# Performance work log

Hardware: AMD Instinct MI355X
Metric: run time of the kernel (lower is better)

## Reference

```python
import jax, jax.numpy as jnp
import numpy as np

B, LP, NC, D, E = 8, 1000, 64, 128, 320  # batch, protein len, compound atoms, hid dim, esm dim


def _linear_params(key, din, dout):
    k1, k2 = jax.random.split(key)
    lim = 1.0 / np.sqrt(din)
    W = jax.random.uniform(k1, (din, dout), minval=-lim, maxval=lim, dtype=jnp.float32)
    b = jax.random.uniform(k2, (dout,), minval=-lim, maxval=lim, dtype=jnp.float32)
    return W, b


def setup_inputs() -> dict:
    key = jax.random.key(0)
    ks = jax.random.split(key, 14)
    inp = {
        "protein_embedding": jax.random.normal(ks[0], (B, LP, E), dtype=jnp.float32),
        "protein_feat_x": jax.random.normal(ks[1], (B, LP, D), dtype=jnp.float32),
        "compound_feats": jax.random.normal(ks[2], (B, NC, D), dtype=jnp.float32),
    }
    layers = [("emb", E, D), ("wq", D, D), ("wk", D, D), ("wv", D, D), ("wo", D, D),
              ("jp", D, D), ("jc", D, D),
              ("c1", D, 1024), ("c2", 1024, 1024), ("c3", 1024, 256), ("c4", 256, 1)]
    for i, (name, din, dout) in enumerate(layers):
        W, b = _linear_params(ks[3 + i], din, dout)
        inp[name + "_w"] = W
        inp[name + "_b"] = b
    return inp


def reference(protein_embedding, protein_feat_x, compound_feats,
              emb_w, emb_b, wq_w, wq_b, wk_w, wk_b, wv_w, wv_b, wo_w, wo_b,
              jp_w, jp_b, jc_w, jc_b,
              c1_w, c1_b, c2_w, c2_b, c3_w, c3_b, c4_w, c4_b):
    # protein sequence embedding -> hid dim
    pe = protein_embedding @ emb_w + emb_b                      # [B, LP, D]
    # single-head cross attention: query = seq embedding, key/value = graph feats
    Q = pe @ wq_w + wq_b
    K = protein_feat_x @ wk_w + wk_b
    V = protein_feat_x @ wv_w + wv_b
    scale = jnp.sqrt(jnp.asarray(D, pe.dtype))                  # n_heads=1 -> head_dim=D
    attn = jax.nn.softmax(jnp.einsum('bqd,bkd->bqk', Q, K) / scale, axis=-1)
    protein_feats = jnp.einsum('bqk,bkd->bqd', attn, V) @ wo_w + wo_b  # [B, LP, D]

    # sigmoid bilinear joint attention over (protein residue, compound atom) pairs
    P = jax.nn.relu(protein_feats) @ jp_w + jp_b                # [B, LP, D]
    C = jax.nn.relu(compound_feats) @ jc_w + jc_b               # [B, NC, D]
    A = jax.nn.sigmoid(jnp.einsum('bid,bkd->bik', P, C))        # [B, LP, NC]
    A = A / jnp.sum(A, axis=(1, 2), keepdims=True)

    # tanh outer product (the costly 4D bikj intermediate) then weighted reduction
    cp = jnp.tanh(protein_feats[:, :, None, :] * compound_feats[:, None, :, :])  # [B, LP, NC, D]
    cp_embedding = jnp.einsum('bikd,bik->bd', cp, A)            # [B, D]

    # classifier MLP (dropout is eval-mode identity)
    h = jax.nn.relu(cp_embedding @ c1_w + c1_b)
    h = jax.nn.relu(h @ c2_w + c2_b)
    h = jax.nn.relu(h @ c3_w + c3_b)
    return h @ c4_w + c4_b                                      # [B, 1]
```

## Files before the change

### kernel.cpp

```cpp
#include <hip/hip_runtime.h>
#include <hip/hip_bf16.h>
#include <math.h>

#define LP 1000
#define NCMP 64
#define NSPLIT 4

typedef _Float16 f16;
typedef f16   v8h __attribute__((ext_vector_type(8)));
typedef float v4f __attribute__((ext_vector_type(4)));

__device__ __forceinline__ float rcp_fast(float x) { return __builtin_amdgcn_rcpf(x); }
__device__ __forceinline__ void fsplit(float x, f16& h, f16& l) {
    h = (f16)x; l = (f16)(x - (float)h);
}
__device__ __forceinline__ void fs8(const float4& f0, const float4& f1, v8h& h, v8h& l) {
    const float x[8] = {f0.x, f0.y, f0.z, f0.w, f1.x, f1.y, f1.z, f1.w};
    #pragma unroll
    for (int i = 0; i < 8; ++i) {
        f16 hh = (f16)x[i];
        h[i] = hh;
        l[i] = (f16)(x[i] - (float)hh);
    }
}

struct H4 { f16 a, b, c, d; };

__device__ __forceinline__ void gemm_core(float (*Ws)[128], float (*Xt)[36],
                                          const float* X, const float* W, const float* bias,
                                          float* Y, int K, int rowbase, bool relu_in)
{
    const int t  = threadIdx.x;
    const int r0 = (t >> 5) * 4;
    const int c0 = (t & 31) * 4;
    const int xr = t >> 3, xk = (t & 7) << 2;
    const int xrow = rowbase + xr;
    float4 xv = *(const float4*)(X + (long)xrow * K + xk);
    float4 wv[4];
    #pragma unroll
    for (int u = 0; u < 4; ++u) {
        int s = t + u * 256, r = s >> 5, cb = (s & 31) << 2;
        wv[u] = *(const float4*)(W + (long)r * 128 + cb);
    }
    float acc[4][4] = {};
    for (int k0 = 0; k0 < K; k0 += 32) {
        float4 xs = xv;
        if (relu_in) { xs.x = fmaxf(xs.x,0.f); xs.y = fmaxf(xs.y,0.f);
                       xs.z = fmaxf(xs.z,0.f); xs.w = fmaxf(xs.w,0.f); }
        Xt[xk+0][xr] = xs.x; Xt[xk+1][xr] = xs.y; Xt[xk+2][xr] = xs.z; Xt[xk+3][xr] = xs.w;
        #pragma unroll
        for (int u = 0; u < 4; ++u) {
            int s = t + u * 256, r = s >> 5, cb = (s & 31) << 2;
            *(float4*)&Ws[r][cb] = wv[u];
        }
        __syncthreads();
        if (k0 + 32 < K) {
            xv = *(const float4*)(X + (long)xrow * K + k0 + 32 + xk);
            #pragma unroll
            for (int u = 0; u < 4; ++u) {
                int s = t + u * 256, r = s >> 5, cb = (s & 31) << 2;
                wv[u] = *(const float4*)(W + (long)(k0 + 32 + r) * 128 + cb);
            }
        }
        #pragma unroll
        for (int kk = 0; kk < 32; ++kk) {
            float4 w4 = *(const float4*)&Ws[kk][c0];
            float4 x4 = *(const float4*)&Xt[kk][r0];
            acc[0][0] = fmaf(x4.x, w4.x, acc[0][0]); acc[0][1] = fmaf(x4.x, w4.y, acc[0][1]);
            acc[0][2] = fmaf(x4.x, w4.z, acc[0][2]); acc[0][3] = fmaf(x4.x, w4.w, acc[0][3]);
            acc[1][0] = fmaf(x4.y, w4.x, acc[1][0]); acc[1][1] = fmaf(x4.y, w4.y, acc[1][1]);
            acc[1][2] = fmaf(x4.y, w4.z, acc[1][2]); acc[1][3] = fmaf(x4.y, w4.w, acc[1][3]);
            acc[2][0] = fmaf(x4.z, w4.x, acc[2][0]); acc[2][1] = fmaf(x4.z, w4.y, acc[2][1]);
            acc[2][2] = fmaf(x4.z, w4.z, acc[2][2]); acc[2][3] = fmaf(x4.z, w4.w, acc[2][3]);
            acc[3][0] = fmaf(x4.w, w4.x, acc[3][0]); acc[3][1] = fmaf(x4.w, w4.y, acc[3][1]);
            acc[3][2] = fmaf(x4.w, w4.z, acc[3][2]); acc[3][3] = fmaf(x4.w, w4.w, acc[3][3]);
        }
        __syncthreads();
    }
    float4 bv = bias ? *(const float4*)(bias + c0) : make_float4(0.f,0.f,0.f,0.f);
    #pragma unroll
    for (int i = 0; i < 4; ++i) {
        int row = rowbase + r0 + i;
        float4 o;
        o.x = acc[i][0] + bv.x; o.y = acc[i][1] + bv.y;
        o.z = acc[i][2] + bv.z; o.w = acc[i][3] + bv.w;
        *(float4*)(Y + (long)row * 128 + c0) = o;
    }
}

__device__ __forceinline__ void gemm_coreT(float (*Ws)[128], float (*Xt)[36],
                                           const float* X, const float* W,
                                           f16* ThT, f16* TlT, int KT, int rowbase)
{
    const int t  = threadIdx.x;
    const int r0 = (t >> 5) * 4;
    const int c0 = (t & 31) * 4;
    const int xr = t >> 3, xk = (t & 7) << 2;
    const int xrow = rowbase + xr;
    float4 xv = *(const float4*)(X + (long)xrow * 128 + xk);
    float4 wv[4];
    #pragma unroll
    for (int u = 0; u < 4; ++u) {
        int s = t + u * 256, r = s >> 5, cb = (s & 31) << 2;
        wv[u] = *(const float4*)(W + (long)r * 128 + cb);
    }
    float acc[4][4] = {};
    for (int k0 = 0; k0 < 128; k0 += 32) {
        Xt[xk+0][xr] = xv.x; Xt[xk+1][xr] = xv.y; Xt[xk+2][xr] = xv.z; Xt[xk+3][xr] = xv.w;
        #pragma unroll
        for (int u = 0; u < 4; ++u) {
            int s = t + u * 256, r = s >> 5, cb = (s & 31) << 2;
            *(float4*)&Ws[r][cb] = wv[u];
        }
        __syncthreads();
        if (k0 + 32 < 128) {
            xv = *(const float4*)(X + (long)xrow * 128 + k0 + 32 + xk);
            #pragma unroll
            for (int u = 0; u < 4; ++u) {
                int s = t + u * 256, r = s >> 5, cb = (s & 31) << 2;
                wv[u] = *(const float4*)(W + (long)(k0 + 32 + r) * 128 + cb);
            }
        }
        #pragma unroll
        for (int kk = 0; kk < 32; ++kk) {
            float4 w4 = *(const float4*)&Ws[kk][c0];
            float4 x4 = *(const float4*)&Xt[kk][r0];
            acc[0][0] = fmaf(x4.x, w4.x, acc[0][0]); acc[0][1] = fmaf(x4.x, w4.y, acc[0][1]);
            acc[0][2] = fmaf(x4.x, w4.z, acc[0][2]); acc[0][3] = fmaf(x4.x, w4.w, acc[0][3]);
            acc[1][0] = fmaf(x4.y, w4.x, acc[1][0]); acc[1][1] = fmaf(x4.y, w4.y, acc[1][1]);
            acc[1][2] = fmaf(x4.y, w4.z, acc[1][2]); acc[1][3] = fmaf(x4.y, w4.w, acc[1][3]);
            acc[2][0] = fmaf(x4.z, w4.x, acc[2][0]); acc[2][1] = fmaf(x4.z, w4.y, acc[2][1]);
            acc[2][2] = fmaf(x4.z, w4.z, acc[2][2]); acc[2][3] = fmaf(x4.z, w4.w, acc[2][3]);
            acc[3][0] = fmaf(x4.w, w4.x, acc[3][0]); acc[3][1] = fmaf(x4.w, w4.y, acc[3][1]);
            acc[3][2] = fmaf(x4.w, w4.z, acc[3][2]); acc[3][3] = fmaf(x4.w, w4.w, acc[3][3]);
        }
        __syncthreads();
    }
    #pragma unroll
    for (int i = 0; i < 4; ++i) {
        int row = rowbase + r0 + i;
        #pragma unroll
        for (int j = 0; j < 4; ++j) {
            f16 h, l; fsplit(acc[i][j], h, l);
            long o = (long)(c0 + j) * KT + row;
            ThT[o] = h; TlT[o] = l;
        }
    }
}

__global__ __launch_bounds__(256) void pre0_k(const float* __restrict__ emb_w, const float* __restrict__ emb_b,
                                              const float* __restrict__ wq_w, const float* __restrict__ wq_b,
                                              const float* __restrict__ wk_w,
                                              const float* __restrict__ wv_w, const float* __restrict__ wv_b,
                                              const float* __restrict__ wo_w, const float* __restrict__ wo_b,
                                              f16* __restrict__ WpThi, f16* __restrict__ WpTlo,
                                              f16* __restrict__ WkThi, f16* __restrict__ WkTlo,
                                              float* __restrict__ bp,
                                              float* __restrict__ Wvo, float* __restrict__ bvo,
                                              float* __restrict__ zbase)
{
    __shared__ __align__(16) float Ws[32][128];
    __shared__ __align__(16) float Xt[32][36];
    const int bid = blockIdx.x;
    const int t = threadIdx.x;
    if (bid < 10) { gemm_coreT(Ws, Xt, emb_w, wq_w, WpThi, WpTlo, 320, bid * 32); return; }
    if (bid >= 11 && bid < 15) { gemm_core(Ws, Xt, wv_w, wo_w, nullptr, Wvo, 128, (bid - 11) * 32, false); return; }
    if (bid >= 16) {
        #pragma unroll
        for (int u = 0; u < 8; ++u) {
            int idx = (bid - 16) * 2048 + u * 256 + t;
            int k = idx >> 7, n = idx & 127;
            f16 h, l; fsplit(wk_w[idx], h, l);
            WkThi[(long)n * 128 + k] = h; WkTlo[(long)n * 128 + k] = l;
        }
        return;
    }
    if (bid == 10 && t >= 128) {
        for (int i = t - 128; i < 1032; i += 128) zbase[i] = 0.f;
        return;
    }
    if (t < 128) {
        const float* vb = (bid == 10) ? emb_b : wv_b;
        const float* Wm = (bid == 10) ? wq_w  : wo_w;
        const float* ab = (bid == 10) ? wq_b  : wo_b;
        float a0 = 0.f, a1 = 0.f, a2 = 0.f, a3 = 0.f;
        for (int k = 0; k < 128; k += 4) {
            a0 = fmaf(vb[k+0], Wm[(k+0)*128 + t], a0);
            a1 = fmaf(vb[k+1], Wm[(k+1)*128 + t], a1);
            a2 = fmaf(vb[k+2], Wm[(k+2)*128 + t], a2);
            a3 = fmaf(vb[k+3], Wm[(k+3)*128 + t], a3);
        }
        float* dst = (bid == 10) ? bp : bvo;
        dst[t] = (a0 + a1) + (a2 + a3) + ab[t];
    }
}

__global__ __launch_bounds__(256) void qkv3_k(
    const float* __restrict__ PE, const float* __restrict__ PFX,
    const f16* __restrict__ WpThi, const f16* __restrict__ WpTlo,
    const f16* __restrict__ WkThi, const f16* __restrict__ WkTlo,
    const float* __restrict__ bp, const float* __restrict__ wk_b,
    const float* __restrict__ CF, const float* __restrict__ jc_w, const float* __restrict__ jc_b,
    f16* __restrict__ Qhi, f16* __restrict__ Qlo,
    f16* __restrict__ Khi, f16* __restrict__ Klo,
    f16* __restrict__ Vthi, f16* __restrict__ Vtlo,
    float* __restrict__ Cj)
{
    __shared__ __align__(16) float Ws[32][128];
    __shared__ __align__(16) float Xt[32][36];
    const int bid = blockIdx.x;
    const int t = threadIdx.x;
    if (bid >= 272) {
        const int rb = (bid - 272) * 32;
        const int d = t >> 1, half = t & 1;
        #pragma unroll 4
        for (int i = 0; i < 16; ++i) {
            int row = rb + half * 16 + i;
            int bb = row / 1000, rr = row - bb * 1000;
            float v = PFX[(long)row * 128 + d];
            f16 h, l; fsplit(v, h, l);
            long o = ((long)bb * 128 + d) * 1024 + rr;
            Vthi[o] = h; Vtlo[o] = l;
        }
        return;
    }
    if (bid >= 256) { gemm_core(Ws, Xt, CF, jc_w, jc_b, Cj, 128, (bid - 256) * 32, true); return; }
    const bool isQ = bid < 128;
    const int b = (bid & 127) >> 4, tile = bid & 15;
    const int KD  = isQ ? 320 : 128;
    const int NCH = isQ ? 10 : 4;
    const float* A = isQ ? PE : PFX;
    const f16* Bhi = isQ ? WpThi : WkThi;
    const f16* Blo = isQ ? WpTlo : WkTlo;
    const float* bias = isQ ? bp : wk_b;
    f16* Yhi = isQ ? Qhi : Khi;
    f16* Ylo = isQ ? Qlo : Klo;

    const int wv = t >> 6, lane = t & 63, quad = lane >> 4, l4 = lane & 15;
    int arow = tile * 64 + wv * 16 + l4; if (arow >= LP) arow = LP - 1;
    const float* a_p = A + ((long)b * LP + arow) * KD;

    v4f acc[8];
    #pragma unroll
    for (int dt = 0; dt < 8; ++dt) acc[dt] = (v4f){0.f, 0.f, 0.f, 0.f};

    for (int kt = 0; kt < NCH; ++kt) {
        const int ko = kt * 32 + quad * 8;
        float4 f0 = *(const float4*)(a_p + ko);
        float4 f1 = *(const float4*)(a_p + ko + 4);
        v8h ah, al;
        fs8(f0, f1, ah, al);
        #pragma unroll
        for (int dt = 0; dt < 8; ++dt) {
            const long bo = (long)(dt * 16 + l4) * KD + ko;
            v8h bh = *(const v8h*)(Bhi + bo);
            v8h bl = *(const v8h*)(Blo + bo);
            acc[dt] = __builtin_amdgcn_mfma_f32_16x16x32_f16(ah, bh, acc[dt], 0, 0, 0);
            acc[dt] = __builtin_amdgcn_mfma_f32_16x16x32_f16(ah, bl, acc[dt], 0, 0, 0);
            acc[dt] = __builtin_amdgcn_mfma_f32_16x16x32_f16(al, bh, acc[dt], 0, 0, 0);
        }
    }
    #pragma unroll
    for (int dt = 0; dt < 8; ++dt) {
        const int col = dt * 16 + l4;
        const float bv = bias[col];
        #pragma unroll
        for (int r = 0; r < 4; ++r) {
            int row = tile * 64 + wv * 16 + quad * 4 + r;
            long o = ((long)b * 1024 + row) * 128 + col;
            f16 h, l; fsplit(acc[dt][r] + bv, h, l);
            Yhi[o] = h; Ylo[o] = l;
        }
    }
}

__global__ __launch_bounds__(256) void flash7_k(const f16* __restrict__ Qhi, const f16* __restrict__ Qlo,
                                                const f16* __restrict__ Khi, const f16* __restrict__ Klo,
                                                const f16* __restrict__ Vthi, const f16* __restrict__ Vtlo,
                                                float* __restrict__ Opart,
                                                float* __restrict__ mpart, float* __restrict__ lpart)
{
    __shared__ __align__(16) f16 KVhi[9216];
    __shared__ __align__(16) f16 KVlo[9216];
    __shared__ __align__(16) f16 Pshi[4][16 * 72];
    __shared__ __align__(16) f16 Pslo[4][16 * 72];
    const int t    = threadIdx.x;
    const int wv   = t >> 6;
    const int lane = t & 63;
    const int quad = lane >> 4;
    const int l4   = lane & 15;
    const int qt = blockIdx.x, sp = blockIdx.y, b = blockIdx.z;
    const int q0 = qt * 64;
    const float SCALE = 0.08838834764831845f;
    const float L2E   = 1.4426950408889634f;

    int qrow = q0 + wv * 16 + l4; if (qrow >= LP) qrow = LP - 1;
    const long qbase = ((long)b * 1024 + qrow) * 128;
    v8h qh[4], ql[4];
    #pragma unroll
    for (int kt4 = 0; kt4 < 4; ++kt4) {
        qh[kt4] = *(const v8h*)(Qhi + qbase + kt4 * 32 + quad * 8);
        ql[kt4] = *(const v8h*)(Qlo + qbase + kt4 * 32 + quad * 8);
    }
    float m_i[4] = { -3.0e38f, -3.0e38f, -3.0e38f, -3.0e38f };
    float l_i[4] = { 0.f, 0.f, 0.f, 0.f };
    v4f  O[8];
    #pragma unroll
    for (int dt = 0; dt < 8; ++dt) O[dt] = (v4f){0.f, 0.f, 0.f, 0.f};

    for (int kt = sp * 4; kt < sp * 4 + 4; ++kt) {
        const int key0 = kt * 64;
        __syncthreads();
        #pragma unroll
        for (int u = 0; u < 4; ++u) {
            int ch = t + u * 256;
            int r = ch >> 4, co = (ch & 15) * 8;
            long ga = ((long)b * 1024 + key0 + r) * 128 + co;
            *(v8h*)(KVhi + r * 136 + co) = *(const v8h*)(Khi + ga);
            *(v8h*)(KVlo + r * 136 + co) = *(const v8h*)(Klo + ga);
        }
        __syncthreads();
        v8h vh[4], vl[4];
        #pragma unroll
        for (int u = 0; u < 4; ++u) {
            int ch = t + u * 256;
            int d = ch >> 3, co = (ch & 7) * 8;
            long ga = ((long)b * 128 + d) * 1024 + key0 + co;
            vh[u] = *(const v8h*)(Vthi + ga);
            vl[u] = *(const v8h*)(Vtlo + ga);
        }
        v4f S[4];
        #pragma unroll
        for (int nt = 0; nt < 4; ++nt) S[nt] = (v4f){0.f, 0.f, 0.f, 0.f};
        #pragma unroll
        for (int nt = 0; nt < 4; ++nt) {
            const int rb = (nt * 16 + l4) * 136;
            #pragma unroll
            for (int kt4 = 0; kt4 < 4; ++kt4) {
                v8h bh = *(const v8h*)(KVhi + rb + kt4 * 32 + quad * 8);
                v8h bl = *(const v8h*)(KVlo + rb + kt4 * 32 + quad * 8);
                S[nt] = __builtin_amdgcn_mfma_f32_16x16x32_f16(qh[kt4], bh, S[nt], 0, 0, 0);
                S[nt] = __builtin_amdgcn_mfma_f32_16x16x32_f16(qh[kt4], bl, S[nt], 0, 0, 0);
                S[nt] = __builtin_amdgcn_mfma_f32_16x16x32_f16(ql[kt4], bh, S[nt], 0, 0, 0);
            }
        }
        #pragma unroll
        for (int nt = 0; nt < 4; ++nt) {
            bool valid = (key0 + nt * 16 + l4) < LP;
            #pragma unroll
            for (int r = 0; r < 4; ++r)
                S[nt][r] = valid ? S[nt][r] * SCALE : -3.0e38f;
        }
        float alpha[4];
        #pragma unroll
        for (int r = 0; r < 4; ++r) {
            float tm = fmaxf(fmaxf(S[0][r], S[1][r]), fmaxf(S[2][r], S[3][r]));
            tm = fmaxf(tm, __shfl_xor(tm, 1));
            tm = fmaxf(tm, __shfl_xor(tm, 2));
            tm = fmaxf(tm, __shfl_xor(tm, 4));
            tm = fmaxf(tm, __shfl_xor(tm, 8));
            float mnew = fmaxf(m_i[r], tm);
            alpha[r] = exp2f((m_i[r] - mnew) * L2E);
            float ps = 0.f;
            #pragma unroll
            for (int nt = 0; nt < 4; ++nt) {
                float p = exp2f((S[nt][r] - mnew) * L2E);
                S[nt][r] = p;
                ps += p;
            }
            ps += __shfl_xor(ps, 1);
            ps += __shfl_xor(ps, 2);
            ps += __shfl_xor(ps, 4);
            ps += __shfl_xor(ps, 8);
            l_i[r] = l_i[r] * alpha[r] + ps;
            m_i[r] = mnew;
        }
        #pragma unroll
        for (int dt = 0; dt < 8; ++dt) {
            O[dt][0] *= alpha[0]; O[dt][1] *= alpha[1];
            O[dt][2] *= alpha[2]; O[dt][3] *= alpha[3];
        }
        __syncthreads();
        #pragma unroll
        for (int u = 0; u < 4; ++u) {
            int ch = t + u * 256;
            int d = ch >> 3, co = (ch & 7) * 8;
            *(v8h*)(KVhi + d * 72 + co) = vh[u];
            *(v8h*)(KVlo + d * 72 + co) = vl[u];
        }
        #pragma unroll
        for (int nt = 0; nt < 4; ++nt) {
            int col = nt * 16 + l4;
            #pragma unroll
            for (int r = 0; r < 4; ++r) {
                f16 ph, pl; fsplit(S[nt][r], ph, pl);
                Pshi[wv][(quad * 4 + r) * 72 + col] = ph;
                Pslo[wv][(quad * 4 + r) * 72 + col] = pl;
            }
        }
        __syncthreads();
        #pragma unroll
        for (int kc = 0; kc < 2; ++kc) {
            v8h pah = *(const v8h*)(Pshi[wv] + l4 * 72 + kc * 32 + quad * 8);
            v8h pal = *(const v8h*)(Pslo[wv] + l4 * 72 + kc * 32 + quad * 8);
            #pragma unroll
            for (int dt = 0; dt < 8; ++dt) {
                v8h vfh = *(const v8h*)(KVhi + (dt * 16 + l4) * 72 + kc * 32 + quad * 8);
                v8h vfl = *(const v8h*)(KVlo + (dt * 16 + l4) * 72 + kc * 32 + quad * 8);
                O[dt] = __builtin_amdgcn_mfma_f32_16x16x32_f16(pah, vfh, O[dt], 0, 0, 0);
                O[dt] = __builtin_amdgcn_mfma_f32_16x16x32_f16(pah, vfl, O[dt], 0, 0, 0);
                O[dt] = __builtin_amdgcn_mfma_f32_16x16x32_f16(pal, vfh, O[dt], 0, 0, 0);
            }
        }
    }
    #pragma unroll
    for (int r = 0; r < 4; ++r) {
        int row = q0 + wv * 16 + quad * 4 + r;
        if (row < LP) {
            long base = (long)sp * 1024000 + ((long)b * LP + row) * 128;
            #pragma unroll
            for (int dt = 0; dt < 8; ++dt)
                Opart[base + dt * 16 + l4] = O[dt][r];
            if (l4 == 0) {
                mpart[(long)sp * 8000 + b * LP + row] = m_i[r];
                lpart[(long)sp * 8000 + b * LP + row] = l_i[r];
            }
        }
    }
}

__global__ __launch_bounds__(256) void mt1ab_k(
    const float* __restrict__ Opart, const float* __restrict__ mp, const float* __restrict__ lp,
    const float* __restrict__ Wvo, const float* __restrict__ bvo,
    const float* __restrict__ jp_w, const float* __restrict__ jp_b,
    float* __restrict__ PF, float* __restrict__ PJ)
{
    __shared__ __align__(16) float Ws[128][128];
    __shared__ __align__(16) float Xs[16][132];
    const int t  = threadIdx.x;
    const int p0 = blockIdx.x * 16;
    const int b  = blockIdx.y;
    const float L2E = 1.4426950408889634f;
    const int r0 = (t >> 5) * 2;
    const int c0 = (t & 31) * 4;

    #pragma unroll
    for (int u = 0; u < 16; ++u) {
        int s = t + u * 256, r = s >> 5, cb = (s & 31) << 2;
        *(float4*)&Ws[r][cb] = *(const float4*)(Wvo + (long)r * 128 + cb);
    }
    {
        const int pr = t >> 4, pc = (t & 15) << 3;
        int grow = p0 + pr; if (grow > LP - 1) grow = LP - 1;
        const long g = (long)b * LP + grow;
        float mm = -3.0e38f;
        #pragma unroll
        for (int s = 0; s < NSPLIT; ++s) mm = fmaxf(mm, mp[g + (long)s * 8000]);
        float wgt[NSPLIT]; float ls = 0.f;
        #pragma unroll
        for (int s = 0; s < NSPLIT; ++s) {
            wgt[s] = exp2f((mp[g + (long)s * 8000] - mm) * L2E);
            ls += wgt[s] * lp[g + (long)s * 8000];
        }
        const float linv = 1.0f / ls;
        float4 a0 = make_float4(0.f,0.f,0.f,0.f), a1 = make_float4(0.f,0.f,0.f,0.f);
        #pragma unroll
        for (int s = 0; s < NSPLIT; ++s) {
            const float* src = Opart + (long)s * 1024000 + g * 128 + pc;
            float4 p = *(const float4*)src;
            float4 q = *(const float4*)(src + 4);
            a0.x = fmaf(wgt[s], p.x, a0.x); a0.y = fmaf(wgt[s], p.y, a0.y);
            a0.z = fmaf(wgt[s], p.z, a0.z); a0.w = fmaf(wgt[s], p.w, a0.w);
            a1.x = fmaf(wgt[s], q.x, a1.x); a1.y = fmaf(wgt[s], q.y, a1.y);
            a1.z = fmaf(wgt[s], q.z, a1.z); a1.w = fmaf(wgt[s], q.w, a1.w);
        }
        *(float4*)&Xs[pr][pc]     = make_float4(a0.x*linv, a0.y*linv, a0.z*linv, a0.w*linv);
        *(float4*)&Xs[pr][pc + 4] = make_float4(a1.x*linv, a1.y*linv, a1.z*linv, a1.w*linv);
    }
    __syncthreads();
    float acc[2][4] = {};
    #pragma unroll 8
    for (int kk4 = 0; kk4 < 128; kk4 += 4) {
        float4 xa = *(const float4*)&Xs[r0 + 0][kk4];
        float4 xb = *(const float4*)&Xs[r0 + 1][kk4];
        #pragma unroll
        for (int j = 0; j < 4; ++j) {
            float4 w4 = *(const float4*)&Ws[kk4 + j][c0];
            float x0 = (j==0)?xa.x:(j==1)?xa.y:(j==2)?xa.z:xa.w;
            float x1 = (j==0)?xb.x:(j==1)?xb.y:(j==2)?xb.z:xb.w;
            acc[0][0]=fmaf(x0,w4.x,acc[0][0]); acc[0][1]=fmaf(x0,w4.y,acc[0][1]);
            acc[0][2]=fmaf(x0,w4.z,acc[0][2]); acc[0][3]=fmaf(x0,w4.w,acc[0][3]);
            acc[1][0]=fmaf(x1,w4.x,acc[1][0]); acc[1][1]=fmaf(x1,w4.y,acc[1][1]);
            acc[1][2]=fmaf(x1,w4.z,acc[1][2]); acc[1][3]=fmaf(x1,w4.w,acc[1][3]);
        }
    }
    __syncthreads();
    #pragma unroll
    for (int u = 0; u < 16; ++u) {
        int s = t + u * 256, r = s >> 5, cb = (s & 31) << 2;
        *(float4*)&Ws[r][cb] = *(const float4*)(jp_w + (long)r * 128 + cb);
    }
    {
        float4 bv = *(const float4*)(bvo + c0);
        #pragma unroll
        for (int i = 0; i < 2; ++i) {
            float4 o = make_float4(acc[i][0]+bv.x, acc[i][1]+bv.y, acc[i][2]+bv.z, acc[i][3]+bv.w);
            int orow = p0 + r0 + i;
            if (orow < LP)
                *(float4*)(PF + ((long)b * LP + orow) * 128 + c0) = o;
            *(float4*)&Xs[r0 + i][c0] =
                make_float4(fmaxf(o.x,0.f), fmaxf(o.y,0.f), fmaxf(o.z,0.f), fmaxf(o.w,0.f));
        }
    }
    __syncthreads();
    float ac2[2][4] = {};
    #pragma unroll 8
    for (int kk4 = 0; kk4 < 128; kk4 += 4) {
        float4 xa = *(const float4*)&Xs[r0 + 0][kk4];
        float4 xb = *(const float4*)&Xs[r0 + 1][kk4];
        #pragma unroll
        for (int j = 0; j < 4; ++j) {
            float4 w4 = *(const float4*)&Ws[kk4 + j][c0];
            float x0 = (j==0)?xa.x:(j==1)?xa.y:(j==2)?xa.z:xa.w;
            float x1 = (j==0)?xb.x:(j==1)?xb.y:(j==2)?xb.z:xb.w;
            ac2[0][0]=fmaf(x0,w4.x,ac2[0][0]); ac2[0][1]=fmaf(x0,w4.y,ac2[0][1]);
            ac2[0][2]=fmaf(x0,w4.z,ac2[0][2]); ac2[0][3]=fmaf(x0,w4.w,ac2[0][3]);
            ac2[1][0]=fmaf(x1,w4.x,ac2[1][0]); ac2[1][1]=fmaf(x1,w4.y,ac2[1][1]);
            ac2[1][2]=fmaf(x1,w4.z,ac2[1][2]); ac2[1][3]=fmaf(x1,w4.w,ac2[1][3]);
        }
    }
    float4 b2 = *(const float4*)(jp_b + c0);
    #pragma unroll
    for (int i = 0; i < 2; ++i) {
        int orow = p0 + r0 + i;
        if (orow < LP)
            *(float4*)(PJ + ((long)b * LP + orow) * 128 + c0) =
                make_float4(ac2[i][0]+b2.x, ac2[i][1]+b2.y, ac2[i][2]+b2.z, ac2[i][3]+b2.w);
    }
}

template<int IIN>
__device__ __forceinline__ float tanh_chunk(const float (*Cs)[132], const float (*AshT)[20],
                                            const float* areg, int d, int kh)
{
    float accD = 0.f;
    for (int kk = 0; kk < 16; ++kk) {
        const int k = (kh << 4) + kk;
        const float cv = Cs[k][d];
        #pragma unroll
        for (int iq = 0; iq < IIN; iq += 4) {
            float4 a4 = *(const float4*)&AshT[k][iq];
            float e0 = exp2f(areg[iq+0] * cv);
            float e1 = exp2f(areg[iq+1] * cv);
            float e2 = exp2f(areg[iq+2] * cv);
            float e3 = exp2f(areg[iq+3] * cv);
            accD = fmaf(1.f - 2.f * rcp_fast(e0 + 1.f), a4.x, accD);
            accD = fmaf(1.f - 2.f * rcp_fast(e1 + 1.f), a4.y, accD);
            accD = fmaf(1.f - 2.f * rcp_fast(e2 + 1.f), a4.z, accD);
            accD = fmaf(1.f - 2.f * rcp_fast(e3 + 1.f), a4.w, accD);
        }
    }
    return accD;
}

__global__ __launch_bounds__(256) void mt2_k(
    const float* __restrict__ PF, const float* __restrict__ PJ,
    const float* __restrict__ Cj, const float* __restrict__ CF,
    float* __restrict__ Asum, float* __restrict__ cpe)
{
    __shared__ __align__(16) float Pjs[16][132];
    __shared__ __align__(16) float Pfs[16][132];
    __shared__ __align__(16) float Cs[32][132];
    __shared__ __align__(16) float AshT[32][20];
    __shared__ float red[256];
    const int t  = threadIdx.x;
    const int p0 = blockIdx.x * 16;
    const int kc = blockIdx.y;
    const int b  = blockIdx.z;
    const float L2E = 1.4426950408889634f;

    {
        int pr = t >> 4, pc = (t & 15) << 3;
        int gr = p0 + pr; if (gr > LP - 1) gr = LP - 1;
        long gb = ((long)b * LP + gr) * 128 + pc;
        *(float4*)&Pjs[pr][pc]     = *(const float4*)(PJ + gb);
        *(float4*)&Pjs[pr][pc + 4] = *(const float4*)(PJ + gb + 4);
        *(float4*)&Pfs[pr][pc]     = *(const float4*)(PF + gb);
        *(float4*)&Pfs[pr][pc + 4] = *(const float4*)(PF + gb + 4);
    }
    float4 cfv[4];
    #pragma unroll
    for (int u = 0; u < 4; ++u) {
        int s = t + u * 256, r = s >> 5, cb = (s & 31) << 2;
        *(float4*)&Cs[r][cb] = *(const float4*)(Cj + ((long)b * NCMP + kc * 32 + r) * 128 + cb);
        cfv[u] = *(const float4*)(CF + ((long)b * NCMP + kc * 32 + r) * 128 + cb);
    }
    __syncthreads();
    const int tr = t >> 4, tc = t & 15;
    float sacc[2] = {0.f, 0.f};
    #pragma unroll 4
    for (int d4 = 0; d4 < 32; ++d4) {
        float4 p4 = *(const float4*)&Pjs[tr][d4 << 2];
        #pragma unroll
        for (int j = 0; j < 2; ++j) {
            float4 cv = *(const float4*)&Cs[tc + (j << 4)][d4 << 2];
            sacc[j] += p4.x*cv.x + p4.y*cv.y + p4.z*cv.z + p4.w*cv.w;
        }
    }
    float lsum = 0.f;
    const int gi = p0 + tr;
    #pragma unroll
    for (int j = 0; j < 2; ++j) {
        float sg = rcp_fast(1.f + exp2f(-sacc[j] * L2E));
        if (gi < LP) { AshT[tc + (j << 4)][tr] = sg; lsum += sg; }
    }
    #pragma unroll
    for (int off = 1; off < 64; off <<= 1) lsum += __shfl_xor(lsum, off);
    if ((t & 63) == 0) red[t >> 6] = lsum;
    __syncthreads();
    if (t == 0) atomicAdd(Asum + b, (red[0] + red[1]) + (red[2] + red[3]));
    #pragma unroll
    for (int u = 0; u < 4; ++u) {
        int s = t + u * 256, r = s >> 5, cb = (s & 31) << 2;
        *(float4*)&Cs[r][cb] = cfv[u];
    }
    __syncthreads();
    const float TWO_L2E = 2.8853900817779268f;
    const int d = t & 127, kh = t >> 7;
    float areg[16];
    #pragma unroll
    for (int ii = 0; ii < 16; ++ii) areg[ii] = Pfs[ii][d] * TWO_L2E;
    float accD = (p0 + 16 <= LP) ? tanh_chunk<16>(Cs, AshT, areg, d, kh)
                                 : tanh_chunk<8>(Cs, AshT, areg, d, kh);
    red[t] = accD;
    __syncthreads();
    if (t < 128) atomicAdd(cpe + (long)b * 128 + t, red[t] + red[t + 128]);
}

__global__ __launch_bounds__(256) void c12_k(const float* __restrict__ cpe, const float* __restrict__ Asum,
                                             const float* __restrict__ c1_w, const float* __restrict__ c1_b,
                                             const float* __restrict__ c2_w, float* __restrict__ part)
{
    __shared__ float sc[8][128];
    __shared__ float ins[8][8];
    const int t = threadIdx.x, ks = blockIdx.x, k0 = ks * 8;
    #pragma unroll
    for (int u = 0; u < 4; ++u) {
        int idx = t + u * 256;
        sc[idx >> 7][idx & 127] = cpe[idx] * rcp_fast(Asum[idx >> 7]);
    }
    __syncthreads();
    if (t < 64) {
        int b = t >> 3, kk = t & 7;
        int n1 = k0 + kk;
        float a0 = 0.f, a1 = 0.f, a2 = 0.f, a3 = 0.f;
        #pragma unroll 8
        for (int j = 0; j < 128; j += 4) {
            a0 = fmaf(sc[b][j+0], c1_w[(long)(j+0)*1024 + n1], a0);
            a1 = fmaf(sc[b][j+1], c1_w[(long)(j+1)*1024 + n1], a1);
            a2 = fmaf(sc[b][j+2], c1_w[(long)(j+2)*1024 + n1], a2);
            a3 = fmaf(sc[b][j+3], c1_w[(long)(j+3)*1024 + n1], a3);
        }
        ins[b][kk] = fmaxf((a0 + a1) + (a2 + a3) + c1_b[n1], 0.f);
    }
    __syncthreads();
    const int n = (t & 63) * 4 + (t >> 6) * 256;
    float4 acc[8] = {};
    #pragma unroll
    for (int kk = 0; kk < 8; ++kk) {
        float4 w4 = *(const float4*)(c2_w + (long)(k0 + kk) * 1024 + n);
        #pragma unroll
        for (int b = 0; b < 8; ++b) {
            float s = ins[b][kk];
            acc[b].x = fmaf(s, w4.x, acc[b].x); acc[b].y = fmaf(s, w4.y, acc[b].y);
            acc[b].z = fmaf(s, w4.z, acc[b].z); acc[b].w = fmaf(s, w4.w, acc[b].w);
        }
    }
    #pragma unroll
    for (int b = 0; b < 8; ++b)
        *(float4*)(part + ((long)(ks * 8 + b)) * 1024 + n) = acc[b];
}

__global__ __launch_bounds__(256) void c3m_k(const float* __restrict__ part2, const float* __restrict__ c2_b,
                                             const float* __restrict__ c3_w, const float* __restrict__ c3_b,
                                             const float* __restrict__ c4_w, const float* __restrict__ c4_b,
                                             float* __restrict__ out)
{
    __shared__ float Hs[1024];
    __shared__ float red[256];
    const int t = threadIdx.x, b = blockIdx.x;
    float4 acc4 = make_float4(0.f,0.f,0.f,0.f);
    #pragma unroll 4
    for (int ks = 0; ks < 128; ++ks) {
        float4 p = *(const float4*)(part2 + ((long)(ks * 8 + b)) * 1024 + t * 4);
        acc4.x += p.x; acc4.y += p.y; acc4.z += p.z; acc4.w += p.w;
    }
    {
        float4 bb = *(const float4*)(c2_b + t * 4);
        Hs[t*4+0] = fmaxf(acc4.x + bb.x, 0.f);
        Hs[t*4+1] = fmaxf(acc4.y + bb.y, 0.f);
        Hs[t*4+2] = fmaxf(acc4.z + bb.z, 0.f);
        Hs[t*4+3] = fmaxf(acc4.w + bb.w, 0.f);
    }
    __syncthreads();
    float a0 = 0.f, a1 = 0.f, a2 = 0.f, a3 = 0.f;
    #pragma unroll 8
    for (int k = 0; k < 1024; k += 4) {
        a0 = fmaf(Hs[k+0], c3_w[(long)(k+0)*256 + t], a0);
        a1 = fmaf(Hs[k+1], c3_w[(long)(k+1)*256 + t], a1);
        a2 = fmaf(Hs[k+2], c3_w[(long)(k+2)*256 + t], a2);
        a3 = fmaf(Hs[k+3], c3_w[(long)(k+3)*256 + t], a3);
    }
    float h3v = fmaxf((a0 + a1) + (a2 + a3) + c3_b[t], 0.f);
    red[t] = h3v * c4_w[t];
    __syncthreads();
    for (int off = 128; off > 0; off >>= 1) {
        if (t < off) red[t] += red[t + off];
        __syncthreads();
    }
    if (t == 0) out[b] = red[0] + c4_b[0];
}

extern "C" void kernel_launch(void* const* d_in, const int* in_sizes, int n_in,
                              void* d_out, int out_size, void* d_ws, size_t ws_size,
                              hipStream_t stream)
{
    const float* PE   = (const float*)d_in[0];
    const float* PFX  = (const float*)d_in[1];
    const float* CF   = (const float*)d_in[2];
    const float* emb_w = (const float*)d_in[3];  const float* emb_b = (const float*)d_in[4];
    const float* wq_w  = (const float*)d_in[5];  const float* wq_b  = (const float*)d_in[6];
    const float* wk_w  = (const float*)d_in[7];  const float* wk_b  = (const float*)d_in[8];
    const float* wv_w  = (const float*)d_in[9];  const float* wv_b  = (const float*)d_in[10];
    const float* wo_w  = (const float*)d_in[11]; const float* wo_b  = (const float*)d_in[12];
    const float* jp_w  = (const float*)d_in[13]; const float* jp_b  = (const float*)d_in[14];
    const float* jc_w  = (const float*)d_in[15]; const float* jc_b  = (const float*)d_in[16];
    const float* c1_w  = (const float*)d_in[17]; const float* c1_b  = (const float*)d_in[18];
    const float* c2_w  = (const float*)d_in[19]; const float* c2_b  = (const float*)d_in[20];
    const float* c3_w  = (const float*)d_in[21]; const float* c3_b  = (const float*)d_in[22];
    const float* c4_w  = (const float*)d_in[23]; const float* c4_b  = (const float*)d_in[24];

    float* ws     = (float*)d_ws;
    f16*  Qhi   = (f16*)ws;
    f16*  Qlo   = (f16*)(ws + 524288);
    f16*  Khi   = (f16*)(ws + 1048576);
    f16*  Klo   = (f16*)(ws + 1572864);
    f16*  Vthi  = (f16*)(ws + 2097152);
    f16*  Vtlo  = (f16*)(ws + 2621440);
    float* bufC   = ws + 3145728;
    float* Opart  = bufC + 65536;
    float* mpart  = Opart + 4096000;
    float* lpart  = mpart + 32000;
    float* Asum   = lpart + 32000;
    float* cpe    = Asum + 8;
    float* bprime = cpe + 1024;
    float* bufWvo = bprime + 128;
    float* bufbvo = bufWvo + 16384;
    float* part2  = ws;
    float* PFbuf  = ws + 1048576;
    float* PJbuf  = ws + 2097152;
    f16* WpThi = (f16*)(ws + 7430144);
    f16* WpTlo = (f16*)(ws + 7450624);
    f16* WkThi = (f16*)(ws + 7471104);
    f16* WkTlo = (f16*)(ws + 7479296);

    pre0_k<<<24, 256, 0, stream>>>(emb_w, emb_b, wq_w, wq_b, wk_w, wv_w, wv_b, wo_w, wo_b,
                                   WpThi, WpTlo, WkThi, WkTlo,
                                   bprime, bufWvo, bufbvo, Asum);
    qkv3_k<<<522, 256, 0, stream>>>(PE, PFX, WpThi, WpTlo, WkThi, WkTlo,
                                    bprime, wk_b, CF, jc_w, jc_b,
                                    Qhi, Qlo, Khi, Klo, Vthi, Vtlo, bufC);
    flash7_k<<<dim3(16, NSPLIT, 8), 256, 0, stream>>>(Qhi, Qlo, Khi, Klo, Vthi, Vtlo,
                                                      Opart, mpart, lpart);
    mt1ab_k<<<dim3(63, 8), 256, 0, stream>>>(Opart, mpart, lpart, bufWvo, bufbvo,
                                             jp_w, jp_b, PFbuf, PJbuf);
    mt2_k<<<dim3(63, 2, 8), 256, 0, stream>>>(PFbuf, PJbuf, bufC, CF, Asum, cpe);
    c12_k<<<128, 256, 0, stream>>>(cpe, Asum, c1_w, c1_b, c2_w, part2);
    c3m_k<<<8, 256, 0, stream>>>(part2, c2_b, c3_w, c3_b, c4_w, c4_b, (float*)d_out);
}
```

Baseline: 273.9 us.

## Split mt2 compound axis into four blocks and read protein rows from global

The tanh outer-product kernel now splits the 64 compound atoms across four blocks of 16 instead of two of 32, doubling the grid to expose more parallelism. Each block also drops the shared-memory staging of the protein rows and reads PJ and PF directly from global memory, which cuts LDS use and improves occupancy. In exchange the protein rows are loaded once per compound split (twice as often overall), there are more atomics into Asum and cpe, and the per-thread inner loop is shorter.

```diff
diff --git a/kernel.cpp b/kernel.cpp
--- a/kernel.cpp
+++ b/kernel.cpp
@@ -544,8 +544,8 @@
                                             const float* areg, int d, int kh)
 {
     float accD = 0.f;
-    for (int kk = 0; kk < 16; ++kk) {
-        const int k = (kh << 4) + kk;
+    for (int kk = 0; kk < 8; ++kk) {
+        const int k = (kh << 3) + kk;
         const float cv = Cs[k][d];
         #pragma unroll
         for (int iq = 0; iq < IIN; iq += 4) {
@@ -568,10 +568,8 @@
     const float* __restrict__ Cj, const float* __restrict__ CF,
     float* __restrict__ Asum, float* __restrict__ cpe)
 {
-    __shared__ __align__(16) float Pjs[16][132];
-    __shared__ __align__(16) float Pfs[16][132];
-    __shared__ __align__(16) float Cs[32][132];
-    __shared__ __align__(16) float AshT[32][20];
+    __shared__ __align__(16) float Cs[16][132];
+    __shared__ __align__(16) float AshT[16][20];
     __shared__ float red[256];
     const int t  = threadIdx.x;
     const int p0 = blockIdx.x * 16;
@@ -579,40 +577,29 @@
     const int b  = blockIdx.z;
     const float L2E = 1.4426950408889634f;
 
-    {
-        int pr = t >> 4, pc = (t & 15) << 3;
-        int gr = p0 + pr; if (gr > LP - 1) gr = LP - 1;
-        long gb = ((long)b * LP + gr) * 128 + pc;
-        *(float4*)&Pjs[pr][pc]     = *(const float4*)(PJ + gb);
-        *(float4*)&Pjs[pr][pc + 4] = *(const float4*)(PJ + gb + 4);
-        *(float4*)&Pfs[pr][pc]     = *(const float4*)(PF + gb);
-        *(float4*)&Pfs[pr][pc + 4] = *(const float4*)(PF + gb + 4);
-    }
-    float4 cfv[4];
-    #pragma unroll
-    for (int u = 0; u < 4; ++u) {
+    float4 cfv[2];
+    #pragma unroll
+    for (int u = 0; u < 2; ++u) {
         int s = t + u * 256, r = s >> 5, cb = (s & 31) << 2;
-        *(float4*)&Cs[r][cb] = *(const float4*)(Cj + ((long)b * NCMP + kc * 32 + r) * 128 + cb);
-        cfv[u] = *(const float4*)(CF + ((long)b * NCMP + kc * 32 + r) * 128 + cb);
+        *(float4*)&Cs[r][cb] = *(const float4*)(Cj + ((long)b * NCMP + kc * 16 + r) * 128 + cb);
+        cfv[u] = *(const float4*)(CF + ((long)b * NCMP + kc * 16 + r) * 128 + cb);
     }
     __syncthreads();
     const int tr = t >> 4, tc = t & 15;
-    float sacc[2] = {0.f, 0.f};
-    #pragma unroll 4
+    int gr = p0 + tr; if (gr > LP - 1) gr = LP - 1;
+    const float* pj = PJ + ((long)b * LP + gr) * 128;
+    float sacc = 0.f;
+    #pragma unroll 8
     for (int d4 = 0; d4 < 32; ++d4) {
-        float4 p4 = *(const float4*)&Pjs[tr][d4 << 2];
-        #pragma unroll
-        for (int j = 0; j < 2; ++j) {
-            float4 cv = *(const float4*)&Cs[tc + (j << 4)][d4 << 2];
-            sacc[j] += p4.x*cv.x + p4.y*cv.y + p4.z*cv.z + p4.w*cv.w;
-        }
+        float4 p4 = *(const float4*)(pj + (d4 << 2));
+        float4 cv = *(const float4*)&Cs[tc][d4 << 2];
+        sacc += p4.x*cv.x + p4.y*cv.y + p4.z*cv.z + p4.w*cv.w;
     }
     float lsum = 0.f;
-    const int gi = p0 + tr;
-    #pragma unroll
-    for (int j = 0; j < 2; ++j) {
-        float sg = rcp_fast(1.f + exp2f(-sacc[j] * L2E));
-        if (gi < LP) { AshT[tc + (j << 4)][tr] = sg; lsum += sg; }
+    if (p0 + tr < LP) {
+        float sg = rcp_fast(1.f + exp2f(-sacc * L2E));
+        AshT[tc][tr] = sg;
+        lsum = sg;
     }
     #pragma unroll
     for (int off = 1; off < 64; off <<= 1) lsum += __shfl_xor(lsum, off);
@@ -620,7 +607,7 @@
     __syncthreads();
     if (t == 0) atomicAdd(Asum + b, (red[0] + red[1]) + (red[2] + red[3]));
     #pragma unroll
-    for (int u = 0; u < 4; ++u) {
+    for (int u = 0; u < 2; ++u) {
         int s = t + u * 256, r = s >> 5, cb = (s & 31) << 2;
         *(float4*)&Cs[r][cb] = cfv[u];
     }
@@ -629,7 +616,10 @@
     const int d = t & 127, kh = t >> 7;
     float areg[16];
     #pragma unroll
-    for (int ii = 0; ii < 16; ++ii) areg[ii] = Pfs[ii][d] * TWO_L2E;
+    for (int ii = 0; ii < 16; ++ii) {
+        int rr = p0 + ii; if (rr > LP - 1) rr = LP - 1;
+        areg[ii] = PF[((long)b * LP + rr) * 128 + d] * TWO_L2E;
+    }
     float accD = (p0 + 16 <= LP) ? tanh_chunk<16>(Cs, AshT, areg, d, kh)
                                  : tanh_chunk<8>(Cs, AshT, areg, d, kh);
     red[t] = accD;
@@ -774,7 +764,7 @@
                                                       Opart, mpart, lpart);
     mt1ab_k<<<dim3(63, 8), 256, 0, stream>>>(Opart, mpart, lpart, bufWvo, bufbvo,
                                              jp_w, jp_b, PFbuf, PJbuf);
-    mt2_k<<<dim3(63, 2, 8), 256, 0, stream>>>(PFbuf, PJbuf, bufC, CF, Asum, cpe);
+    mt2_k<<<dim3(63, 4, 8), 256, 0, stream>>>(PFbuf, PJbuf, bufC, CF, Asum, cpe);
     c12_k<<<128, 256, 0, stream>>>(cpe, Asum, c1_w, c1_b, c2_w, part2);
     c3m_k<<<8, 256, 0, stream>>>(part2, c2_b, c3_w, c3_b, c4_w, c4_b, (float*)d_out);
 }
```

Result: slower. 296.3 us (+8.2%).
